# Kernel optimization log

Measured on AMD Instinct MI355X. Metric: run time of the kernel, lower is better.

The kernel has to match this reference:

```python
import jax, jax.numpy as jnp
import numpy as np

N_NODES = 100000
N_EDGES = 3200000
N_GRAPHS = 512
D_FEAT = 128


def spmm(edge_index, edge_weight, h, n_nodes):
    # out_i = sum_{(i,j) in E} w_ij * h_j   (row = edge_index[0], col = edge_index[1])
    row, col = edge_index[0], edge_index[1]
    msgs = edge_weight[:, None] * h[col]            # [E, F]
    return jax.ops.segment_sum(msgs, row, num_segments=n_nodes)


def gcn_conv(x, edge_index, edge_weight, W, b):
    h = x @ W                                       # project first (Spektral order)
    h = spmm(edge_index, edge_weight, h, x.shape[0]) + b
    return jax.nn.elu(h)


def setup_inputs() -> dict:
    key = jax.random.key(0)
    ks = jax.random.split(key, 12)
    x = jax.random.normal(ks[0], (N_NODES, D_FEAT), dtype=jnp.float32)
    edge_index = jax.random.randint(ks[1], (2, N_EDGES), 0, N_NODES, dtype=jnp.int32)
    edge_weight = jax.random.uniform(ks[2], (N_EDGES,), dtype=jnp.float32)
    seg_ids = jnp.sort(jax.random.randint(ks[3], (N_NODES,), 0, N_GRAPHS, dtype=jnp.int32))
    s = 0.1
    return {
        "x": x,
        "edge_index": edge_index,
        "edge_weight": edge_weight,
        "seg_ids": seg_ids,
        "W1": jax.random.normal(ks[4], (D_FEAT, 32), dtype=jnp.float32) * s,
        "b1": jnp.zeros((32,), jnp.float32),
        "W2": jax.random.normal(ks[5], (32, 32), dtype=jnp.float32) * s,
        "b2": jnp.zeros((32,), jnp.float32),
        "W3": jax.random.normal(ks[6], (32, 32), dtype=jnp.float32) * s,
        "b3": jnp.zeros((32,), jnp.float32),
        "Wd1": jax.random.normal(ks[7], (32, 64), dtype=jnp.float32) * s,
        "bd1": jnp.zeros((64,), jnp.float32),
        "Wd2": jax.random.normal(ks[8], (64, 32), dtype=jnp.float32) * s,
        "bd2": jnp.zeros((32,), jnp.float32),
        "Wd3": jax.random.normal(ks[9], (32, 1), dtype=jnp.float32) * s,
        "bd3": jnp.zeros((1,), jnp.float32),
    }


def reference(x, edge_index, edge_weight, seg_ids, W1, b1, W2, b2, W3, b3,
              Wd1, bd1, Wd2, bd2, Wd3, bd3):
    h = gcn_conv(x, edge_index, edge_weight, W1, b1)
    h = gcn_conv(h, edge_index, edge_weight, W2, b2)
    h = gcn_conv(h, edge_index, edge_weight, W3, b3)
    # GlobalSumPool over graph index (disjoint mode)
    g = jax.ops.segment_sum(h, seg_ids, num_segments=N_GRAPHS)  # [G, 32]
    g = jax.nn.relu(g @ Wd1 + bd1)   # dropout = identity at inference
    g = jax.nn.relu(g @ Wd2 + bd2)
    out = jax.nn.sigmoid(g @ Wd3 + bd3)  # [G, 1]
    return out
```

## Files before the change

kernel.cpp:

```cpp
#include <hip/hip_runtime.h>
#include <hip/hip_fp16.h>
#include <math.h>

#define N_NODES 100000
#define N_EDGES 3200000
#define N_GRAPHS 512
#define D_FEAT 128
#define F_HID 32

#define RPB 128
#define NB 782
#define CAP 5120
#define CHUNK 8192
#define SBS 1024
#define NCHUNK ((N_EDGES + CHUNK - 1) / CHUNK)
#define CTILES 16
#define NKEYS (RPB * CTILES)
#define SPB 64

static __device__ __forceinline__ __half2 u2h2(unsigned u) {
    return *reinterpret_cast<__half2*>(&u);
}

__global__ void gemm128x32(const float* __restrict__ x, const float* __restrict__ W,
                           unsigned short* __restrict__ outh, int n_nodes) {
    __shared__ float Ws[128 * 32];
    for (int i = threadIdx.x; i < 128 * 32; i += 256) Ws[i] = W[i];
    __syncthreads();
    const int fg = threadIdx.x & 7;
    const int nl = threadIdx.x >> 3;
    const int node = blockIdx.x * 32 + nl;
    if (node >= n_nodes) return;
    const float4* x4 = (const float4*)(x + (size_t)node * 128);
    const float4* Ws4 = (const float4*)Ws;
    float4 acc = make_float4(0.f, 0.f, 0.f, 0.f);
    for (int kk = 0; kk < 32; ++kk) {
        float4 xv = x4[kk];
        int k = kk * 4;
        float4 w0 = Ws4[(k + 0) * 8 + fg];
        float4 w1 = Ws4[(k + 1) * 8 + fg];
        float4 w2 = Ws4[(k + 2) * 8 + fg];
        float4 w3 = Ws4[(k + 3) * 8 + fg];
        acc.x += xv.x * w0.x + xv.y * w1.x + xv.z * w2.x + xv.w * w3.x;
        acc.y += xv.x * w0.y + xv.y * w1.y + xv.z * w2.y + xv.w * w3.y;
        acc.z += xv.x * w0.z + xv.y * w1.z + xv.z * w2.z + xv.w * w3.z;
        acc.w += xv.x * w0.w + xv.y * w1.w + xv.z * w2.w + xv.w * w3.w;
    }
    __half2 p0 = __floats2half2_rn(acc.x, acc.y);
    __half2 p1 = __floats2half2_rn(acc.z, acc.w);
    uint2 o = make_uint2(*reinterpret_cast<unsigned*>(&p0),
                         *reinterpret_cast<unsigned*>(&p1));
    ((uint2*)(outh + (size_t)node * 32))[fg] = o;
}

__global__ void init_cursor(int* __restrict__ cursor) {
    int t = blockIdx.x * blockDim.x + threadIdx.x;
    if (t < NB) cursor[t] = t * CAP;
}

__global__ __launch_bounds__(SBS) void bucket_scatter(
        const int* __restrict__ row, const int* __restrict__ col,
        const float* __restrict__ w, int* __restrict__ cursor,
        uint2* __restrict__ rec, int n_edges) {
    __shared__ uint2 srt[CHUNK];
    __shared__ int hist[NB];
    __shared__ int lofs[NB + 1];
    __shared__ int lbase[NB];
    __shared__ int tsum[SBS];
    __shared__ unsigned short flr[CHUNK / 16];
    const int t = threadIdx.x;
    const int base = blockIdx.x * CHUNK;
    const int count = min(CHUNK, n_edges - base);

    if (t < NB) hist[t] = 0;
    __syncthreads();
    int rloc[CHUNK / SBS];
    #pragma unroll
    for (int j = 0; j < CHUNK / SBS; ++j) {
        int i = t + j * SBS;
        int r = -1;
        if (i < count) { r = row[base + i]; atomicAdd(&hist[r >> 7], 1); }
        rloc[j] = r;
    }
    __syncthreads();
    int v = (t < NB) ? hist[t] : 0;
    tsum[t] = v;
    __syncthreads();
    for (int off = 1; off < SBS; off <<= 1) {
        int add = (t >= off) ? tsum[t - off] : 0;
        __syncthreads();
        tsum[t] += add;
        __syncthreads();
    }
    if (t < NB) lofs[t] = tsum[t] - v;
    if (t == SBS - 1) lofs[NB] = tsum[SBS - 1];
    __syncthreads();
    if (t < NB) {
        lbase[t] = v ? atomicAdd(&cursor[t], v) : 0;
        hist[t] = 0;
    }
    for (int q = t; q < CHUNK / 16; q += SBS) {
        int pos = q * 16;
        int lo = 0, hi = NB;
        while (hi - lo > 1) {
            int mid = (lo + hi) >> 1;
            if (lofs[mid] <= pos) lo = mid; else hi = mid;
        }
        flr[q] = (unsigned short)lo;
    }
    __syncthreads();
    #pragma unroll
    for (int j = 0; j < CHUNK / SBS; ++j) {
        int i = t + j * SBS;
        if (i < count) {
            int e = base + i;
            int r = rloc[j];
            int b = r >> 7;
            int pos = lofs[b] + atomicAdd(&hist[b], 1);
            srt[pos] = make_uint2(((unsigned)(r & 127) << 17) | (unsigned)col[e],
                                  __float_as_uint(w[e]));
        }
    }
    __syncthreads();
    for (int i = t; i < count; i += SBS) {
        uint2 vv = srt[i];
        int b = flr[i >> 4];
        while (lofs[b + 1] <= i) ++b;
        rec[lbase[b] + (i - lofs[b])] = vv;
    }
}

__global__ void scan_nb(const int* __restrict__ cursor, int* __restrict__ bbase) {
    __shared__ int s[1024];
    const int t = threadIdx.x;
    int v = (t < NB) ? (cursor[t] - t * CAP) : 0;
    s[t] = v;
    __syncthreads();
    for (int off = 1; off < 1024; off <<= 1) {
        int add = (t >= off) ? s[t - off] : 0;
        __syncthreads();
        s[t] += add;
        __syncthreads();
    }
    if (t < NB) bbase[t] = s[t] - v;
    if (t == NB - 1) bbase[NB] = s[t];
}

__global__ __launch_bounds__(512) void bucket_sort(
        const int* __restrict__ cursor, const int* __restrict__ bbase,
        const uint2* __restrict__ rec, unsigned* __restrict__ rec2,
        int* __restrict__ row_ptr, int n_nodes) {
    __shared__ unsigned srt[CAP];
    __shared__ int hist[NKEYS];
    __shared__ int lofs[NKEYS];
    __shared__ int tsum[512];
    const int t = threadIdx.x;
    const int b = blockIdx.x;
    const int sbase = b * CAP;
    const int cnt = cursor[b] - sbase;
    const int gbase = bbase[b];

    for (int i = t; i < NKEYS; i += 512) hist[i] = 0;
    __syncthreads();
    for (int i = t; i < cnt; i += 512) {
        unsigned rx = rec[sbase + i].x;
        int key = (rx >> 17) * CTILES + ((rx & 0x1FFFFu) >> 13);
        atomicAdd(&hist[key], 1);
    }
    __syncthreads();
    int vals[4];
    int s0 = 0;
    const int k4 = t * 4;
    #pragma unroll
    for (int j = 0; j < 4; ++j) { vals[j] = hist[k4 + j]; s0 += vals[j]; }
    tsum[t] = s0;
    __syncthreads();
    for (int off = 1; off < 512; off <<= 1) {
        int add = (t >= off) ? tsum[t - off] : 0;
        __syncthreads();
        tsum[t] += add;
        __syncthreads();
    }
    {
        int run = tsum[t] - s0;
        #pragma unroll
        for (int j = 0; j < 4; ++j) { lofs[k4 + j] = run; run += vals[j]; }
    }
    __syncthreads();
    if (t < RPB) {
        int gr = b * RPB + t;
        if (gr <= n_nodes) row_ptr[gr] = gbase + lofs[t * CTILES];
    }
    for (int i = t; i < NKEYS; i += 512) hist[i] = lofs[i];
    __syncthreads();
    for (int i = t; i < cnt; i += 512) {
        uint2 v = rec[sbase + i];
        int key = (v.x >> 17) * CTILES + ((v.x & 0x1FFFFu) >> 13);
        int pos = atomicAdd(&hist[key], 1);
        float wf = __uint_as_float(v.y);
        __half hw = __float2half_rn(wf);
        unsigned wb = ((unsigned)*reinterpret_cast<unsigned short*>(&hw)) & 0x7FFFu;
        srt[pos] = (wb << 17) | (v.x & 0x1FFFFu);
    }
    __syncthreads();
    for (int i = t; i < cnt; i += 512)
        rec2[gbase + i] = srt[i];
}

__global__ __launch_bounds__(256) void spmm_fused(
        const int* __restrict__ rp, const unsigned* __restrict__ rec2,
        const unsigned short* __restrict__ h_in, const float* __restrict__ bias,
        const float* __restrict__ Wn,
        unsigned short* __restrict__ h_out,
        const int* __restrict__ seg,
        float* __restrict__ G,
        int n_nodes) {
    __shared__ float Ws[32 * 32];
    __shared__ float vt[SPB][33];
    const int t = threadIdx.x;
    if (Wn) for (int i = t; i < 1024; i += 256) Ws[i] = Wn[i];
    const int fl = t & 3;
    const int nl = t >> 2;
    const int node = blockIdx.x * SPB + nl;
    const bool valid = node < n_nodes;
    const int s = valid ? rp[node] : 0;
    const int e = valid ? rp[node + 1] : 0;
    const uint4* h4 = (const uint4*)h_in;
    __half2 a0 = u2h2(0), a1 = u2h2(0), a2 = u2h2(0), a3 = u2h2(0);
    int i = s;
    for (; i < e && (i & 3); ++i) {
        unsigned p0 = rec2[i];
        uint4 g0 = h4[(size_t)(p0 & 0x1FFFF) * 4 + fl];
        unsigned wu = p0 >> 17; wu |= wu << 16;
        __half2 w2 = u2h2(wu);
        a0 = __hfma2(w2, u2h2(g0.x), a0);
        a1 = __hfma2(w2, u2h2(g0.y), a1);
        a2 = __hfma2(w2, u2h2(g0.z), a2);
        a3 = __hfma2(w2, u2h2(g0.w), a3);
    }
    for (; i + 8 <= e; i += 8) {
        uint4 pa = *(const uint4*)(rec2 + i);
        uint4 pb = *(const uint4*)(rec2 + i + 4);
        unsigned p[8] = {pa.x, pa.y, pa.z, pa.w, pb.x, pb.y, pb.z, pb.w};
        uint4 g[8];
        #pragma unroll
        for (int j = 0; j < 8; ++j) g[j] = h4[(size_t)(p[j] & 0x1FFFF) * 4 + fl];
        #pragma unroll
        for (int j = 0; j < 8; ++j) {
            unsigned wu = p[j] >> 17; wu |= wu << 16;
            __half2 w2 = u2h2(wu);
            a0 = __hfma2(w2, u2h2(g[j].x), a0);
            a1 = __hfma2(w2, u2h2(g[j].y), a1);
            a2 = __hfma2(w2, u2h2(g[j].z), a2);
            a3 = __hfma2(w2, u2h2(g[j].w), a3);
        }
    }
    for (; i < e; ++i) {
        unsigned p0 = rec2[i];
        uint4 g0 = h4[(size_t)(p0 & 0x1FFFF) * 4 + fl];
        unsigned wu = p0 >> 17; wu |= wu << 16;
        __half2 w2 = u2h2(wu);
        a0 = __hfma2(w2, u2h2(g0.x), a0);
        a1 = __hfma2(w2, u2h2(g0.y), a1);
        a2 = __hfma2(w2, u2h2(g0.z), a2);
        a3 = __hfma2(w2, u2h2(g0.w), a3);
    }
    float acc[8];
    acc[0] = __low2float(a0); acc[1] = __high2float(a0);
    acc[2] = __low2float(a1); acc[3] = __high2float(a1);
    acc[4] = __low2float(a2); acc[5] = __high2float(a2);
    acc[6] = __low2float(a3); acc[7] = __high2float(a3);
    float4 bv0 = ((const float4*)bias)[fl * 2];
    float4 bv1 = ((const float4*)bias)[fl * 2 + 1];
    acc[0] += bv0.x; acc[1] += bv0.y; acc[2] += bv0.z; acc[3] += bv0.w;
    acc[4] += bv1.x; acc[5] += bv1.y; acc[6] += bv1.z; acc[7] += bv1.w;
    #pragma unroll
    for (int j = 0; j < 8; ++j)
        acc[j] = acc[j] > 0.f ? acc[j] : (expf(acc[j]) - 1.f);
    {
        float* vr = &vt[nl][fl * 8];
        #pragma unroll
        for (int j = 0; j < 8; ++j) vr[j] = acc[j];
    }
    __syncthreads();

    if (Wn) {
        const float4* Ws4 = (const float4*)Ws;
        const float* vrow = vt[nl];
        float o[8] = {0.f, 0.f, 0.f, 0.f, 0.f, 0.f, 0.f, 0.f};
        #pragma unroll 8
        for (int k = 0; k < 32; ++k) {
            float vk = vrow[k];
            float4 w0 = Ws4[k * 8 + fl * 2];
            float4 w1 = Ws4[k * 8 + fl * 2 + 1];
            o[0] += vk * w0.x; o[1] += vk * w0.y; o[2] += vk * w0.z; o[3] += vk * w0.w;
            o[4] += vk * w1.x; o[5] += vk * w1.y; o[6] += vk * w1.z; o[7] += vk * w1.w;
        }
        if (valid) {
            __half2 q0 = __floats2half2_rn(o[0], o[1]);
            __half2 q1 = __floats2half2_rn(o[2], o[3]);
            __half2 q2 = __floats2half2_rn(o[4], o[5]);
            __half2 q3 = __floats2half2_rn(o[6], o[7]);
            uint4 ob = make_uint4(*reinterpret_cast<unsigned*>(&q0),
                                  *reinterpret_cast<unsigned*>(&q1),
                                  *reinterpret_cast<unsigned*>(&q2),
                                  *reinterpret_cast<unsigned*>(&q3));
            ((uint4*)h_out)[(size_t)node * 4 + fl] = ob;
        }
    } else {
        const int f = t & 31;
        const int sub = t >> 5;
        float run = 0.f;
        int cur = -1;
        #pragma unroll
        for (int q = 0; q < 8; ++q) {
            int nloc = sub * 8 + q;
            int node2 = blockIdx.x * SPB + nloc;
            if (node2 >= n_nodes) break;
            int sg = seg[node2];
            if (sg != cur) {
                if (cur >= 0) atomicAdd(&G[(size_t)cur * 32 + f], run);
                cur = sg;
                run = 0.f;
            }
            run += vt[nloc][f];
        }
        if (cur >= 0) atomicAdd(&G[(size_t)cur * 32 + f], run);
    }
}

__global__ void head_mlp(const float* __restrict__ g,
                         const float* __restrict__ Wd1, const float* __restrict__ bd1,
                         const float* __restrict__ Wd2, const float* __restrict__ bd2,
                         const float* __restrict__ Wd3, const float* __restrict__ bd3,
                         float* __restrict__ out) {
    __shared__ float gr[32];
    __shared__ float s1[64];
    __shared__ float s2[32];
    const int gid = blockIdx.x;
    const int t = threadIdx.x;
    if (t < 32) gr[t] = g[(size_t)gid * 32 + t];
    __syncthreads();
    float a = bd1[t];
    for (int k = 0; k < 32; ++k) a += gr[k] * Wd1[k * 64 + t];
    s1[t] = fmaxf(a, 0.f);
    __syncthreads();
    if (t < 32) {
        float a2 = bd2[t];
        for (int k = 0; k < 64; ++k) a2 += s1[k] * Wd2[k * 32 + t];
        s2[t] = fmaxf(a2, 0.f);
    }
    __syncthreads();
    if (t == 0) {
        float a3 = bd3[0];
        for (int k = 0; k < 32; ++k) a3 += s2[k] * Wd3[k];
        out[gid] = 1.f / (1.f + expf(-a3));
    }
}

extern "C" void kernel_launch(void* const* d_in, const int* in_sizes, int n_in,
                              void* d_out, int out_size, void* d_ws, size_t ws_size,
                              hipStream_t stream) {
    const float* x   = (const float*)d_in[0];
    const int*   ei  = (const int*)d_in[1];
    const float* ew  = (const float*)d_in[2];
    const int*   seg = (const int*)d_in[3];
    const float* W1  = (const float*)d_in[4];
    const float* b1  = (const float*)d_in[5];
    const float* W2  = (const float*)d_in[6];
    const float* b2  = (const float*)d_in[7];
    const float* W3  = (const float*)d_in[8];
    const float* b3  = (const float*)d_in[9];
    const float* Wd1 = (const float*)d_in[10];
    const float* bd1 = (const float*)d_in[11];
    const float* Wd2 = (const float*)d_in[12];
    const float* bd2 = (const float*)d_in[13];
    const float* Wd3 = (const float*)d_in[14];
    const float* bd3 = (const float*)d_in[15];
    float* out = (float*)d_out;

    const int* rowp = ei;
    const int* colp = ei + N_EDGES;

    const size_t NF  = (size_t)N_NODES * F_HID;
    const size_t REC_BYTES = (size_t)NB * CAP * sizeof(uint2);

    char*  wsb     = (char*)d_ws;
    uint2* rec     = (uint2*)wsb;
    unsigned short* hA = (unsigned short*)wsb;
    unsigned short* hB = (unsigned short*)(wsb + NF * 2);
    unsigned* rec2 = (unsigned*)(wsb + REC_BYTES);
    int*   cursor  = (int*)(rec2 + N_EDGES);
    int*   bbase   = cursor + NB;
    int*   row_ptr = bbase + NB + 1;
    float* G       = (float*)(row_ptr + N_NODES + 1);

    const int gemm_grid = (N_NODES + 31) / 32;
    const int spmm_grid = (N_NODES + SPB - 1) / SPB;

    init_cursor<<<(NB + 255) / 256, 256, 0, stream>>>(cursor);
    bucket_scatter<<<NCHUNK, SBS, 0, stream>>>(rowp, colp, ew, cursor, rec, N_EDGES);
    scan_nb<<<1, 1024, 0, stream>>>(cursor, bbase);
    bucket_sort<<<NB, 512, 0, stream>>>(cursor, bbase, rec, rec2, row_ptr, N_NODES);
    hipMemsetAsync(G, 0, (size_t)N_GRAPHS * F_HID * sizeof(float), stream);

    gemm128x32<<<gemm_grid, 256, 0, stream>>>(x, W1, hA, N_NODES);
    spmm_fused<<<spmm_grid, 256, 0, stream>>>(row_ptr, rec2, hA, b1, W2, hB, nullptr, nullptr, N_NODES);

    spmm_fused<<<spmm_grid, 256, 0, stream>>>(row_ptr, rec2, hB, b2, W3, hA, nullptr, nullptr, N_NODES);

    spmm_fused<<<spmm_grid, 256, 0, stream>>>(row_ptr, rec2, hA, b3, nullptr, nullptr, seg, G, N_NODES);

    head_mlp<<<N_GRAPHS, 64, 0, stream>>>(G, Wd1, bd1, Wd2, bd2, Wd3, bd3, out);
}
```

Before: 196.0 us.

## Split each node's edge list across two thread groups in fused SpMM

The fused SpMM kernel now gives each node 8 threads instead of 4. Each half of the threads gathers half of the node's edges, and the two partial sums are combined through shared memory before the bias and ELU are applied. The next-layer projection then runs with each thread computing 4 output features, and each block covers 32 nodes instead of 64. This doubles the memory-level parallelism per node to hide gather latency, and adds an occupancy hint, in exchange for an extra shared-memory reduction and barrier and more blocks.

New measurement: 197.2 us. Within noise of the previous version (+0.6%).

```diff
diff --git a/kernel.cpp b/kernel.cpp
--- a/kernel.cpp
+++ b/kernel.cpp
@@ -16,7 +16,7 @@
 #define NCHUNK ((N_EDGES + CHUNK - 1) / CHUNK)
 #define CTILES 16
 #define NKEYS (RPB * CTILES)
-#define SPB 64
+#define SPB 32
 
 static __device__ __forceinline__ __half2 u2h2(unsigned u) {
     return *reinterpret_cast<__half2*>(&u);
@@ -207,7 +207,7 @@
         rec2[gbase + i] = srt[i];
 }
 
-__global__ __launch_bounds__(256) void spmm_fused(
+__global__ __launch_bounds__(256, 6) void spmm_fused(
         const int* __restrict__ rp, const unsigned* __restrict__ rec2,
         const unsigned short* __restrict__ h_in, const float* __restrict__ bias,
         const float* __restrict__ Wn,
@@ -216,19 +216,25 @@
         float* __restrict__ G,
         int n_nodes) {
     __shared__ float Ws[32 * 32];
-    __shared__ float vt[SPB][33];
+    __shared__ float vt[SPB][84];
     const int t = threadIdx.x;
     if (Wn) for (int i = t; i < 1024; i += 256) Ws[i] = Wn[i];
     const int fl = t & 3;
-    const int nl = t >> 2;
+    const int hf = (t >> 2) & 1;
+    const int nl = t >> 3;
+    const int l8 = t & 7;
     const int node = blockIdx.x * SPB + nl;
     const bool valid = node < n_nodes;
-    const int s = valid ? rp[node] : 0;
-    const int e = valid ? rp[node + 1] : 0;
+    int s = 0, e = 0;
+    if (valid) { s = rp[node]; e = rp[node + 1]; }
+    const int cnt = e - s;
+    const int hl = (cnt + 1) >> 1;
+    int i  = s + hf * hl;
+    const int hiE = hf ? e : (s + hl);
     const uint4* h4 = (const uint4*)h_in;
     __half2 a0 = u2h2(0), a1 = u2h2(0), a2 = u2h2(0), a3 = u2h2(0);
-    int i = s;
-    for (; i < e && (i & 3); ++i) {
+
+    for (; i < hiE && (i & 3); ++i) {
         unsigned p0 = rec2[i];
         uint4 g0 = h4[(size_t)(p0 & 0x1FFFF) * 4 + fl];
         unsigned wu = p0 >> 17; wu |= wu << 16;
@@ -238,7 +244,7 @@
         a2 = __hfma2(w2, u2h2(g0.z), a2);
         a3 = __hfma2(w2, u2h2(g0.w), a3);
     }
-    for (; i + 8 <= e; i += 8) {
+    for (; i + 8 <= hiE; i += 8) {
         uint4 pa = *(const uint4*)(rec2 + i);
         uint4 pb = *(const uint4*)(rec2 + i + 4);
         unsigned p[8] = {pa.x, pa.y, pa.z, pa.w, pb.x, pb.y, pb.z, pb.w};
@@ -255,7 +261,24 @@
             a3 = __hfma2(w2, u2h2(g[j].w), a3);
         }
     }
-    for (; i < e; ++i) {
+    if (i + 4 <= hiE) {
+        uint4 pa = *(const uint4*)(rec2 + i);
+        unsigned p[4] = {pa.x, pa.y, pa.z, pa.w};
+        uint4 g[4];
+        #pragma unroll
+        for (int j = 0; j < 4; ++j) g[j] = h4[(size_t)(p[j] & 0x1FFFF) * 4 + fl];
+        #pragma unroll
+        for (int j = 0; j < 4; ++j) {
+            unsigned wu = p[j] >> 17; wu |= wu << 16;
+            __half2 w2 = u2h2(wu);
+            a0 = __hfma2(w2, u2h2(g[j].x), a0);
+            a1 = __hfma2(w2, u2h2(g[j].y), a1);
+            a2 = __hfma2(w2, u2h2(g[j].z), a2);
+            a3 = __hfma2(w2, u2h2(g[j].w), a3);
+        }
+        i += 4;
+    }
+    for (; i < hiE; ++i) {
         unsigned p0 = rec2[i];
         uint4 g0 = h4[(size_t)(p0 & 0x1FFFF) * 4 + fl];
         unsigned wu = p0 >> 17; wu |= wu << 16;
@@ -265,47 +288,50 @@
         a2 = __hfma2(w2, u2h2(g0.z), a2);
         a3 = __hfma2(w2, u2h2(g0.w), a3);
     }
-    float acc[8];
-    acc[0] = __low2float(a0); acc[1] = __high2float(a0);
-    acc[2] = __low2float(a1); acc[3] = __high2float(a1);
-    acc[4] = __low2float(a2); acc[5] = __high2float(a2);
-    acc[6] = __low2float(a3); acc[7] = __high2float(a3);
-    float4 bv0 = ((const float4*)bias)[fl * 2];
-    float4 bv1 = ((const float4*)bias)[fl * 2 + 1];
-    acc[0] += bv0.x; acc[1] += bv0.y; acc[2] += bv0.z; acc[3] += bv0.w;
-    acc[4] += bv1.x; acc[5] += bv1.y; acc[6] += bv1.z; acc[7] += bv1.w;
-    #pragma unroll
-    for (int j = 0; j < 8; ++j)
-        acc[j] = acc[j] > 0.f ? acc[j] : (expf(acc[j]) - 1.f);
+
     {
-        float* vr = &vt[nl][fl * 8];
-        #pragma unroll
-        for (int j = 0; j < 8; ++j) vr[j] = acc[j];
+        float4 s0 = make_float4(__low2float(a0), __high2float(a0),
+                                __low2float(a1), __high2float(a1));
+        float4 s1 = make_float4(__low2float(a2), __high2float(a2),
+                                __low2float(a3), __high2float(a3));
+        float* vr = &vt[nl][hf * 40 + fl * 8];
+        *(float4*)vr = s0;
+        *(float4*)(vr + 4) = s1;
+    }
+    __syncthreads();
+
+    {
+        float4 b4 = ((const float4*)bias)[l8];
+        float4 p0 = *(const float4*)&vt[nl][l8 * 4];
+        float4 p1 = *(const float4*)&vt[nl][40 + l8 * 4];
+        float r0 = p0.x + p1.x + b4.x;
+        float r1 = p0.y + p1.y + b4.y;
+        float r2 = p0.z + p1.z + b4.z;
+        float r3 = p0.w + p1.w + b4.w;
+        r0 = r0 > 0.f ? r0 : (expf(r0) - 1.f);
+        r1 = r1 > 0.f ? r1 : (expf(r1) - 1.f);
+        r2 = r2 > 0.f ? r2 : (expf(r2) - 1.f);
+        r3 = r3 > 0.f ? r3 : (expf(r3) - 1.f);
+        *(float4*)&vt[nl][l8 * 4] = make_float4(r0, r1, r2, r3);
     }
     __syncthreads();
 
     if (Wn) {
         const float4* Ws4 = (const float4*)Ws;
         const float* vrow = vt[nl];
-        float o[8] = {0.f, 0.f, 0.f, 0.f, 0.f, 0.f, 0.f, 0.f};
+        float4 o = make_float4(0.f, 0.f, 0.f, 0.f);
         #pragma unroll 8
         for (int k = 0; k < 32; ++k) {
             float vk = vrow[k];
-            float4 w0 = Ws4[k * 8 + fl * 2];
-            float4 w1 = Ws4[k * 8 + fl * 2 + 1];
-            o[0] += vk * w0.x; o[1] += vk * w0.y; o[2] += vk * w0.z; o[3] += vk * w0.w;
-            o[4] += vk * w1.x; o[5] += vk * w1.y; o[6] += vk * w1.z; o[7] += vk * w1.w;
+            float4 w = Ws4[k * 8 + l8];
+            o.x += vk * w.x; o.y += vk * w.y; o.z += vk * w.z; o.w += vk * w.w;
         }
         if (valid) {
-            __half2 q0 = __floats2half2_rn(o[0], o[1]);
-            __half2 q1 = __floats2half2_rn(o[2], o[3]);
-            __half2 q2 = __floats2half2_rn(o[4], o[5]);
-            __half2 q3 = __floats2half2_rn(o[6], o[7]);
-            uint4 ob = make_uint4(*reinterpret_cast<unsigned*>(&q0),
-                                  *reinterpret_cast<unsigned*>(&q1),
-                                  *reinterpret_cast<unsigned*>(&q2),
-                                  *reinterpret_cast<unsigned*>(&q3));
-            ((uint4*)h_out)[(size_t)node * 4 + fl] = ob;
+            __half2 q0 = __floats2half2_rn(o.x, o.y);
+            __half2 q1 = __floats2half2_rn(o.z, o.w);
+            uint2 ob = make_uint2(*reinterpret_cast<unsigned*>(&q0),
+                                  *reinterpret_cast<unsigned*>(&q1));
+            ((uint2*)h_out)[(size_t)node * 8 + l8] = ob;
         }
     } else {
         const int f = t & 31;
@@ -313,8 +339,8 @@
         float run = 0.f;
         int cur = -1;
         #pragma unroll
-        for (int q = 0; q < 8; ++q) {
-            int nloc = sub * 8 + q;
+        for (int q = 0; q < 4; ++q) {
+            int nloc = sub * 4 + q;
             int node2 = blockIdx.x * SPB + nloc;
             if (node2 >= n_nodes) break;
             int sg = seg[node2];
```
